# Optimization experiments

Hardware: AMD Instinct MI355X
Metric: run time of the kernel (lower is better)

Reference implementation:

```python
import jax, jax.numpy as jnp
import numpy as np

DIM = 128
P = (2, 2, 2)
D_STATE = 8
D_CONV = 4
EXPAND = 2
D_INNER = EXPAND * DIM
DT_RANK = (DIM + 15) // 16  # ceil(d_model/16) = 8
EPS = 1e-5


def setup_inputs() -> dict:
    key = jax.random.key(0)
    ks = jax.random.split(key, 8)
    B, C, Z, H, W = 2, DIM, 40, 40, 40
    s = lambda k, shape, scale: jax.random.normal(k, shape, jnp.float32) * scale
    return {
        "x": jax.random.normal(ks[0], (B, C, Z, H, W), jnp.float32),
        "norm_g": jnp.ones((C,), jnp.float32),
        "norm_b": jnp.zeros((C,), jnp.float32),
        "in_proj_w": s(ks[1], (2 * D_INNER, C), 0.02),
        "conv_w": s(ks[2], (D_INNER, D_CONV), 0.1),
        "conv_b": jnp.zeros((D_INNER,), jnp.float32),
        "x_proj_w": s(ks[3], (DT_RANK + 2 * D_STATE, D_INNER), 0.02),
        "dt_proj_w": s(ks[4], (D_INNER, DT_RANK), 0.1),
        # softplus^-1(0.01): small positive init for delta, as in mamba_ssm
        "dt_bias": jnp.log(jnp.expm1(jnp.full((D_INNER,), 0.01, jnp.float32))),
        # S4D-real init: A_log = log([1..d_state]) per channel
        "A_log": jnp.log(jnp.tile(jnp.arange(1, D_STATE + 1, dtype=jnp.float32), (D_INNER, 1))),
        "D_vec": jnp.ones((D_INNER,), jnp.float32),
        "out_proj_w": s(ks[5], (DIM, D_INNER), 0.02),
    }


def _mamba(xn, in_proj_w, conv_w, conv_b, x_proj_w, dt_proj_w, dt_bias, A_log, D_vec, out_proj_w):
    # xn: (NB, L, C)
    NB, L, _ = xn.shape
    xz = jnp.einsum('blc,ec->ble', xn, in_proj_w)          # (NB, L, 2*d_inner)
    xp, z = jnp.split(xz, 2, axis=-1)
    # causal depthwise conv1d, kernel D_CONV, truncated to L
    xpad = jnp.pad(xp, ((0, 0), (D_CONV - 1, 0), (0, 0)))
    conv = conv_b
    for k in range(D_CONV):
        conv = conv + xpad[:, k:k + L, :] * conv_w[:, k]
    u = jax.nn.silu(conv)                                  # (NB, L, d_inner)
    xdbl = jnp.einsum('bld,ed->ble', u, x_proj_w)
    dt, Bm, Cm = jnp.split(xdbl, [DT_RANK, DT_RANK + D_STATE], axis=-1)
    delta = jax.nn.softplus(jnp.einsum('blr,dr->bld', dt, dt_proj_w) + dt_bias)
    A = -jnp.exp(A_log)                                    # (d_inner, d_state)

    def step(h, inp):
        d_t, B_t, C_t, u_t = inp  # (NB,d_inner),(NB,d_state),(NB,d_state),(NB,d_inner)
        h = jnp.exp(d_t[:, :, None] * A) * h + (d_t * u_t)[:, :, None] * B_t[:, None, :]
        return h, jnp.einsum('bds,bs->bd', h, C_t)

    h0 = jnp.zeros((NB, D_INNER, D_STATE), xn.dtype)
    xs = (jnp.swapaxes(delta, 0, 1), jnp.swapaxes(Bm, 0, 1),
          jnp.swapaxes(Cm, 0, 1), jnp.swapaxes(u, 0, 1))
    _, ys = jax.lax.scan(step, h0, xs)                     # ys: (L, NB, d_inner)
    y = jnp.swapaxes(ys, 0, 1) + u * D_vec
    y = y * jax.nn.silu(z)
    return jnp.einsum('bld,cd->blc', y, out_proj_w)        # (NB, L, C)


def reference(x, norm_g, norm_b, in_proj_w, conv_w, conv_b, x_proj_w, dt_proj_w,
              dt_bias, A_log, D_vec, out_proj_w):
    B, C, Z, H, W = x.shape
    p1, p2, p3 = P
    NZ, NH, NW = Z // p1, H // p2, W // p3
    NB, L = B * p1 * p2 * p3, NZ * NH * NW
    # patch reshuffle: (B,C,Z,H,W) -> (B*p1*p2*p3, C, NZ, NH, NW)
    xd = x.reshape(B, C, NZ, p1, NH, p2, NW, p3).transpose(0, 3, 5, 7, 1, 2, 4, 6)
    xf = jnp.swapaxes(xd.reshape(NB, C, L), 1, 2)          # (NB, L, C)
    # LayerNorm over channel dim
    mu = xf.mean(-1, keepdims=True)
    var = xf.var(-1, keepdims=True)
    xn = (xf - mu) * jax.lax.rsqrt(var + EPS) * norm_g + norm_b
    yo = _mamba(xn, in_proj_w, conv_w, conv_b, x_proj_w, dt_proj_w, dt_bias,
                A_log, D_vec, out_proj_w)                  # (NB, L, C)
    # undo reshuffle
    xo = jnp.swapaxes(yo, 1, 2).reshape(B, p1, p2, p3, C, NZ, NH, NW)
    xo = xo.transpose(0, 4, 5, 1, 6, 2, 7, 3).reshape(B, C, Z, H, W)
    return xo + x
```

## Files before the change

### kernel.cpp

```cpp
#include <hip/hip_runtime.h>

#define NBATCH 16
#define LSEQ   8000
#define MROWS  128000
#define CDIM   128
#define DI     256
#define DS     8
#define DTR    8
#define NXP    24
#define NC     250
#define CL     32

#define OFF_PB    0ull
#define OFF_XN    1024000ull
#define OFF_STA   1024000ull
#define OFF_XP    33792000ull
#define OFF_XDBL  33792000ull
#define OFF_STH   46080000ull
#define OFF_ZS    99328000ull
#define OFF_U     164864000ull
#define WS_NEEDED 230400000ull

#define P_G    0
#define P_B    128
#define P_IPW  256
#define P_CW   65792
#define P_CB   66816
#define P_XPW  67072
#define P_DTW  73216
#define P_DTB  75264
#define P_ALOG 75520
#define P_DVEC 77568
#define P_OPW  77824
#define P_TOT  110592

typedef __attribute__((ext_vector_type(8))) short bf16x8;
typedef __attribute__((ext_vector_type(4))) float f32x4;
typedef __attribute__((ext_vector_type(2))) float f32x2;

__device__ __forceinline__ float bf2f(unsigned short a) {
    union { unsigned int u; float f; } v; v.u = ((unsigned int)a) << 16; return v.f;
}
__device__ __forceinline__ unsigned short f2bf(float f) {
    union { float f; unsigned int u; } v; v.f = f;
    unsigned int r = v.u + 0x7FFFu + ((v.u >> 16) & 1u);
    return (unsigned short)(r >> 16);
}
__device__ __forceinline__ unsigned short f2bf_cvt(float f) {
    unsigned int r;
    asm("v_cvt_pk_bf16_f32 %0, %1, %2" : "=v"(r) : "v"(f), "v"(0.f));
    return (unsigned short)r;
}
__device__ __forceinline__ bool bfmode(const void* g) {
    return ((const unsigned int*)g)[0] == 0x3F803F80u;
}
__device__ __forceinline__ float rd(const void* p, size_t i, bool bf) {
    return bf ? bf2f(((const unsigned short*)p)[i]) : ((const float*)p)[i];
}
__device__ __forceinline__ f32x2 pk_fma(f32x2 a, f32x2 b, f32x2 c) {
    f32x2 d;
    asm("v_pk_fma_f32 %0, %1, %2, %3" : "=v"(d) : "v"(a), "v"(b), "v"(c));
    return d;
}
__device__ __forceinline__ f32x2 pk_mul(f32x2 a, f32x2 b) {
    f32x2 d;
    asm("v_pk_mul_f32 %0, %1, %2" : "=v"(d) : "v"(a), "v"(b));
    return d;
}
__device__ __forceinline__ int m_of(int b, int sp) {
    int z = sp / 1600;
    int rem = sp - z * 1600;
    int h = rem / 40;
    int w = rem - h * 40;
    int nb = b * 8 + (z & 1) * 4 + (h & 1) * 2 + (w & 1);
    int l = (z >> 1) * 400 + (h >> 1) * 20 + (w >> 1);
    return nb * LSEQ + l;
}

__global__ __launch_bounds__(256) void param_convert(const void* g, const void* b, const void* ipw,
                                                     const void* cw, const void* cb, const void* xpw,
                                                     const void* dtw, const void* dtb, const void* alog,
                                                     const void* dvec, const void* opw,
                                                     unsigned short* __restrict__ pb)
{
    int gid = blockIdx.x * 256 + threadIdx.x;
    if (gid >= P_TOT) return;
    bool bf = bfmode(g);
    const void* src; int off;
    if      (gid < P_B)    { src = g;    off = P_G; }
    else if (gid < P_IPW)  { src = b;    off = P_B; }
    else if (gid < P_CW)   { src = ipw;  off = P_IPW; }
    else if (gid < P_CB)   { src = cw;   off = P_CW; }
    else if (gid < P_XPW)  { src = cb;   off = P_CB; }
    else if (gid < P_DTW)  { src = xpw;  off = P_XPW; }
    else if (gid < P_DTB)  { src = dtw;  off = P_DTW; }
    else if (gid < P_ALOG) { src = dtb;  off = P_DTB; }
    else if (gid < P_DVEC) { src = alog; off = P_ALOG; }
    else if (gid < P_OPW)  { src = dvec; off = P_DVEC; }
    else                   { src = opw;  off = P_OPW; }
    pb[gid] = f2bf(rd(src, gid - off, bf));
}

__global__ __launch_bounds__(256) void lnorm_kernel(const void* __restrict__ x,
                                                    const unsigned short* __restrict__ pb,
                                                    unsigned short* __restrict__ xn)
{
    __shared__ float tile[128][65];
    __shared__ float psum[4][64], psqs[4][64];
    __shared__ float smu[64], srs[64];
    int b  = blockIdx.y;
    int sp0 = blockIdx.x * 64;
    int t = threadIdx.x;

    int spi = t & 63, cpart = t >> 6;
    const float* xf = (const float*)x;
#pragma unroll
    for (int pass = 0; pass < 32; ++pass) {
        int c = pass * 4 + cpart;
        tile[c][spi] = xf[((size_t)b * CDIM + c) * 64000 + sp0 + spi];
    }
    __syncthreads();

    {
        float s = 0.f, ss = 0.f;
        int c0 = cpart * 32;
#pragma unroll
        for (int cc = 0; cc < 32; ++cc) {
            float v = tile[c0 + cc][spi];
            s += v; ss += v * v;
        }
        psum[cpart][spi] = s; psqs[cpart][spi] = ss;
    }
    __syncthreads();
    if (cpart == 0) {
        float s  = psum[0][spi] + psum[1][spi] + psum[2][spi] + psum[3][spi];
        float ss = psqs[0][spi] + psqs[1][spi] + psqs[2][spi] + psqs[3][spi];
        float m = s * (1.f / CDIM);
        float var = ss * (1.f / CDIM) - m * m;
        smu[spi] = m;
        srs[spi] = rsqrtf(var + 1e-5f);
    }
    __syncthreads();

    int c = t & 127, half = t >> 7;
    float gc = bf2f(pb[P_G + c]), bc = bf2f(pb[P_B + c]);
#pragma unroll
    for (int pass = 0; pass < 32; ++pass) {
        int j = pass * 2 + half;
        int m = m_of(b, sp0 + j);
        float v = (tile[c][j] - smu[j]) * srs[j] * gc + bc;
        xn[(size_t)m * CDIM + c] = f2bf(v);
    }
}

__global__ __launch_bounds__(256) void gemm_bt_kernel(const unsigned short* __restrict__ A,
                                                      const unsigned short* __restrict__ W,
                                                      void* __restrict__ D,
                                                      int K, int Nact, int ldd, int act)
{
    __shared__ unsigned short As[128 * 32];
    __shared__ unsigned short Ws[128 * 32];
    int tid = threadIdx.x;
    int m0 = blockIdx.x * 128;
    int n0 = blockIdx.y * 128;
    int wave = tid >> 6, lane = tid & 63;
    int wm = (wave & 1) * 64, wn = (wave >> 1) * 64;
    int lrow = lane & 15, lk = (lane >> 4) * 8;
    int quad = lane >> 4;

    f32x4 acc[4][4];
#pragma unroll
    for (int i = 0; i < 4; i++)
#pragma unroll
        for (int j = 0; j < 4; j++) acc[i][j] = (f32x4){0.f, 0.f, 0.f, 0.f};

    int rowA0 = tid >> 2, kcA0 = (tid & 3) << 3;
    int rowA1 = (tid + 256) >> 2, kcA1 = (tid & 3) << 3;

    for (int kt = 0; kt < K; kt += 32) {
        *(uint4*)&As[rowA0 * 32 + kcA0] = *(const uint4*)&A[(size_t)(m0 + rowA0) * K + kt + kcA0];
        *(uint4*)&As[rowA1 * 32 + kcA1] = *(const uint4*)&A[(size_t)(m0 + rowA1) * K + kt + kcA1];
        uint4 z4 = {0u, 0u, 0u, 0u};
        uint4 w0 = (n0 + rowA0 < Nact) ? *(const uint4*)&W[(size_t)(n0 + rowA0) * K + kt + kcA0] : z4;
        uint4 w1 = (n0 + rowA1 < Nact) ? *(const uint4*)&W[(size_t)(n0 + rowA1) * K + kt + kcA1] : z4;
        *(uint4*)&Ws[rowA0 * 32 + kcA0] = w0;
        *(uint4*)&Ws[rowA1 * 32 + kcA1] = w1;
        __syncthreads();

        bf16x8 af[4], bfr[4];
#pragma unroll
        for (int i = 0; i < 4; i++) af[i]  = *(const bf16x8*)&As[(wm + i * 16 + lrow) * 32 + lk];
#pragma unroll
        for (int j = 0; j < 4; j++) bfr[j] = *(const bf16x8*)&Ws[(wn + j * 16 + lrow) * 32 + lk];
#pragma unroll
        for (int i = 0; i < 4; i++)
#pragma unroll
            for (int j = 0; j < 4; j++)
                acc[i][j] = __builtin_amdgcn_mfma_f32_16x16x32_bf16(af[i], bfr[j], acc[i][j], 0, 0, 0);
        __syncthreads();
    }

#pragma unroll
    for (int i = 0; i < 4; i++)
#pragma unroll
        for (int j = 0; j < 4; j++) {
            int n = n0 + wn + j * 16 + lrow;
            if (n < Nact) {
#pragma unroll
                for (int r = 0; r < 4; r++) {
                    int m = m0 + wm + i * 16 + quad * 4 + r;
                    float v = acc[i][j][r];
                    if (act == 1) v = v / (1.f + __expf(-v));
                    ((unsigned short*)D)[(size_t)m * ldd + n] = f2bf(v);
                }
            }
        }
}

__global__ __launch_bounds__(256) void gemm_conv_kernel(const unsigned short* __restrict__ A,
                                                        const unsigned short* __restrict__ W,
                                                        const unsigned short* __restrict__ cw,
                                                        const unsigned short* __restrict__ cb,
                                                        unsigned short* __restrict__ u)
{
    __shared__ unsigned short As[128 * 32];
    __shared__ unsigned short Ws[128 * 32];
    __shared__ unsigned short Dt[128 * 132];

    int tid = threadIdx.x;
    int tile = blockIdx.x & 63;
    int nb = blockIdx.x >> 6;
    int n0 = blockIdx.y * 128;
    int m0 = nb * 8000 + tile * 125;
    int mA = m0 - 3;
    int wave = tid >> 6, lane = tid & 63;
    int wm = (wave & 1) * 64, wn = (wave >> 1) * 64;
    int lrow = lane & 15, lk = (lane >> 4) * 8;
    int quad = lane >> 4;

    f32x4 acc[4][4];
#pragma unroll
    for (int i = 0; i < 4; i++)
#pragma unroll
        for (int j = 0; j < 4; j++) acc[i][j] = (f32x4){0.f, 0.f, 0.f, 0.f};

    int rowA0 = tid >> 2, kcA0 = (tid & 3) << 3;
    int rowA1 = (tid + 256) >> 2;

    for (int kt = 0; kt < CDIM; kt += 32) {
        uint4 z4 = {0u, 0u, 0u, 0u};
        uint4 a0 = (tile == 0 && rowA0 < 3) ? z4
                 : *(const uint4*)&A[(size_t)(mA + rowA0) * CDIM + kt + kcA0];
        uint4 a1 = *(const uint4*)&A[(size_t)(mA + rowA1) * CDIM + kt + kcA0];
        *(uint4*)&As[rowA0 * 32 + kcA0] = a0;
        *(uint4*)&As[rowA1 * 32 + kcA0] = a1;
        *(uint4*)&Ws[rowA0 * 32 + kcA0] = *(const uint4*)&W[(size_t)(n0 + rowA0) * CDIM + kt + kcA0];
        *(uint4*)&Ws[rowA1 * 32 + kcA0] = *(const uint4*)&W[(size_t)(n0 + rowA1) * CDIM + kt + kcA0];
        __syncthreads();

        bf16x8 af[4], bfr[4];
#pragma unroll
        for (int i = 0; i < 4; i++) af[i]  = *(const bf16x8*)&As[(wm + i * 16 + lrow) * 32 + lk];
#pragma unroll
        for (int j = 0; j < 4; j++) bfr[j] = *(const bf16x8*)&Ws[(wn + j * 16 + lrow) * 32 + lk];
#pragma unroll
        for (int i = 0; i < 4; i++)
#pragma unroll
            for (int j = 0; j < 4; j++)
                acc[i][j] = __builtin_amdgcn_mfma_f32_16x16x32_bf16(af[i], bfr[j], acc[i][j], 0, 0, 0);
        __syncthreads();
    }

#pragma unroll
    for (int i = 0; i < 4; i++)
#pragma unroll
        for (int j = 0; j < 4; j++) {
            int nl = wn + j * 16 + lrow;
            int tr = wm + i * 16 + quad * 4;
            unsigned int c01, c23;
            asm("v_cvt_pk_bf16_f32 %0, %1, %2" : "=v"(c01) : "v"(acc[i][j][0]), "v"(acc[i][j][1]));
            asm("v_cvt_pk_bf16_f32 %0, %1, %2" : "=v"(c23) : "v"(acc[i][j][2]), "v"(acc[i][j][3]));
            *(unsigned int*)&Dt[nl * 132 + tr]     = c01;
            *(unsigned int*)&Dt[nl * 132 + tr + 2] = c23;
        }
    __syncthreads();

    {
        int nl = tid & 127, half = tid >> 7;
        int dch = n0 + nl;
        float cw0 = bf2f(cw[dch * 4 + 0]), cw1 = bf2f(cw[dch * 4 + 1]);
        float cw2 = bf2f(cw[dch * 4 + 2]), cw3 = bf2f(cw[dch * 4 + 3]);
        float cbv = bf2f(cb[dch]);
        int tr0 = half ? 66 : 3;
        int nsteps = half ? 62 : 63;
        const unsigned short* col = &Dt[nl * 132];
        float x0 = bf2f(col[tr0 - 3]), x1 = bf2f(col[tr0 - 2]), x2 = bf2f(col[tr0 - 1]);
        unsigned short* uout = &u[(size_t)(m0 + tr0 - 3) * DI + dch];
#pragma unroll 1
        for (int k = 0; k < nsteps; ++k) {
            float x3 = bf2f(col[tr0 + k]);
            float a = cbv + cw0 * x0 + cw1 * x1 + cw2 * x2 + cw3 * x3;
            float uv = a * __builtin_amdgcn_rcpf(1.f + __expf(-a));
            *uout = f2bf_cvt(uv);
            uout += DI;
            x0 = x1; x1 = x2; x2 = x3;
        }
    }
}


#define BODY1(UR, RO) do {                                                       \
    union { f32x4 q; f32x2 h[2]; } qa, qb, qc, qd;                               \
    qa.q = *(const f32x4*)(rfp + (RO));                                          \
    qb.q = *(const f32x4*)(rfp + (RO) + 4);                                      \
    qc.q = *(const f32x4*)(rfp + (RO) + 8);                                      \
    qd.q = *(const f32x4*)(rfp + (RO) + 12);                                     \
    f32x2 din2 = pk_fma(qa.h[0], Wq[0], bias2);                                  \
    din2 = pk_fma(qa.h[1], Wq[1], din2);                                         \
    din2 = pk_fma(qb.h[0], Wq[2], din2);                                         \
    din2 = pk_fma(qb.h[1], Wq[3], din2);                                         \
    float din = din2.x + din2.y;                                                 \
    float e = __expf(din);                                                       \
    float w = 1.f + e;                                                           \
    float p1 = __builtin_amdgcn_rcpf(w);                                         \
    float delta = (din > 15.f) ? din : __logf(w);                                \
    float du = delta * bf2f(UR);                                                 \
    float p2 = p1 * p1;                                                          \
    f32x2 q1; q1.x = p1; q1.y = p2;                                              \
    f32x2 pp2; pp2.x = p2; pp2.y = p2;                                           \
    f32x2 q2 = pk_mul(q1, pp2);                                                  \
    f32x2 pp4; pp4.x = q2.y; pp4.y = q2.y;                                       \
    f32x2 q3 = pk_mul(q1, pp4);                                                  \
    f32x2 q4 = pk_mul(q2, pp4);                                                  \
    f32x2 du2; du2.x = du; du2.y = du;                                           \
    h2[0] = pk_fma(du2, qc.h[0], pk_mul(q1, h2[0]));                             \
    h2[1] = pk_fma(du2, qc.h[1], pk_mul(q2, h2[1]));                             \
    h2[2] = pk_fma(du2, qd.h[0], pk_mul(q3, h2[2]));                             \
    h2[3] = pk_fma(du2, qd.h[1], pk_mul(q4, h2[3]));                             \
    P *= p1;                                                                     \
} while (0)

__global__ __launch_bounds__(256) void gemm_xdbl_scan1(const unsigned short* __restrict__ u,
                                                       const unsigned short* __restrict__ W,
                                                       const unsigned short* __restrict__ dtw,
                                                       const unsigned short* __restrict__ dtb,
                                                       const unsigned short* __restrict__ alog,
                                                       float* __restrict__ xdbl,
                                                       float* __restrict__ stA,
                                                       float* __restrict__ stH)
{
    __shared__ unsigned short As[128 * 32];
    __shared__ unsigned short Ws[128 * 32];
    __shared__ float Dxs[128 * NXP];
    int tid = threadIdx.x;
    int m0 = blockIdx.x * 128;
    int wave = tid >> 6, lane = tid & 63;
    int wm = (wave & 1) * 64, wn = (wave >> 1) * 64;
    int lrow = lane & 15, lk = (lane >> 4) * 8;
    int quad = lane >> 4;

    f32x4 acc[4][4];
#pragma unroll
    for (int i = 0; i < 4; i++)
#pragma unroll
        for (int j = 0; j < 4; j++) acc[i][j] = (f32x4){0.f, 0.f, 0.f, 0.f};

    int rowA0 = tid >> 2, kcA0 = (tid & 3) << 3;
    int rowA1 = (tid + 256) >> 2;

    for (int kt = 0; kt < DI; kt += 32) {
        *(uint4*)&As[rowA0 * 32 + kcA0] = *(const uint4*)&u[(size_t)(m0 + rowA0) * DI + kt + kcA0];
        *(uint4*)&As[rowA1 * 32 + kcA0] = *(const uint4*)&u[(size_t)(m0 + rowA1) * DI + kt + kcA0];
        uint4 z4 = {0u, 0u, 0u, 0u};
        uint4 w0 = (rowA0 < NXP) ? *(const uint4*)&W[(size_t)rowA0 * DI + kt + kcA0] : z4;
        *(uint4*)&Ws[rowA0 * 32 + kcA0] = w0;
        *(uint4*)&Ws[rowA1 * 32 + kcA0] = z4;
        __syncthreads();

        bf16x8 af[4], bfr[4];
#pragma unroll
        for (int i = 0; i < 4; i++) af[i]  = *(const bf16x8*)&As[(wm + i * 16 + lrow) * 32 + lk];
#pragma unroll
        for (int j = 0; j < 4; j++) bfr[j] = *(const bf16x8*)&Ws[(wn + j * 16 + lrow) * 32 + lk];
#pragma unroll
        for (int i = 0; i < 4; i++)
#pragma unroll
            for (int j = 0; j < 4; j++)
                acc[i][j] = __builtin_amdgcn_mfma_f32_16x16x32_bf16(af[i], bfr[j], acc[i][j], 0, 0, 0);
        __syncthreads();
    }

#pragma unroll
    for (int i = 0; i < 4; i++)
#pragma unroll
        for (int j = 0; j < 4; j++) {
            int n = wn + j * 16 + lrow;
            if (n < NXP) {
#pragma unroll
                for (int r = 0; r < 4; r++) {
                    int ml = wm + i * 16 + quad * 4 + r;
                    float v = acc[i][j][r];
                    xdbl[(size_t)(m0 + ml) * NXP + n] = v;
                    Dxs[ml * NXP + n] = v;
                }
            }
        }
    __syncthreads();

    int d = tid;
    f32x2 Wq[4];
#pragma unroll
    for (int r = 0; r < 4; r++) {
        Wq[r].x = bf2f(dtw[d * DTR + 2 * r]);
        Wq[r].y = bf2f(dtw[d * DTR + 2 * r + 1]);
    }
    float Av[DS];
#pragma unroll
    for (int s = 0; s < DS; s++) Av[s] = -__expf(bf2f(alog[d * DS + s]));
    float A1 = Av[0];
    bool fast = (A1 == -1.0f);
#pragma unroll
    for (int s = 1; s < DS; s++)
        fast = fast && (fabsf(Av[s] - (float)(s + 1) * A1) <= 0.02f * (float)(s + 1) * fabsf(A1));
    float bias = bf2f(dtb[d]);
    f32x2 bias2; bias2.x = bias; bias2.y = 0.f;

#pragma unroll 1
    for (int k = 0; k < 4; ++k) {
        int gm0 = m0 + 32 * k;
        int nb = gm0 / 8000;
        int cc = (gm0 - nb * 8000) >> 5;
        size_t o = (((size_t)cc * NBATCH + nb) * DI + d) * DS;
        const unsigned short* up = u + (size_t)gm0 * DI + d;
        const float* rfp = &Dxs[32 * k * NXP];

        if (fast) {
            f32x2 h2[4];
#pragma unroll
            for (int i = 0; i < 4; i++) { h2[i].x = 0.f; h2[i].y = 0.f; }
            float P = 1.f;
            unsigned short u0 = up[0], u1 = up[DI];
            const unsigned short* uld = up + 2 * DI;
#pragma unroll 1
            for (int t = 0; t < CL - 2; t += 2) {
                unsigned short ua = uld[0], ub = uld[DI]; uld += 2 * DI;
                BODY1(u0, 0);
                BODY1(u1, NXP);
                u0 = ua; u1 = ub;
                rfp += 2 * NXP;
            }
            BODY1(u0, 0);
            BODY1(u1, NXP);
            float P2 = P * P, P3 = P2 * P, P4 = P2 * P2;
            float apv[DS] = {P, P2, P3, P4, P4 * P, P3 * P3, P4 * P3, P4 * P4};
#pragma unroll
            for (int s = 0; s < DS; s++) stA[o + s] = apv[s];
#pragma unroll
            for (int i = 0; i < 4; i++) { stH[o + 2 * i] = h2[i].x; stH[o + 2 * i + 1] = h2[i].y; }
        } else {
            float Wdt[DTR];
#pragma unroll
            for (int r = 0; r < 4; r++) { Wdt[2 * r] = Wq[r].x; Wdt[2 * r + 1] = Wq[r].y; }
            float h[DS], ap[DS];
#pragma unroll
            for (int s = 0; s < DS; s++) { h[s] = 0.f; ap[s] = 1.f; }
            const unsigned short* uld = up;
#pragma unroll 1
            for (int t = 0; t < CL; ++t) {
                float uv = bf2f(*uld); uld += DI;
                float din = bias;
#pragma unroll
                for (int r = 0; r < DTR; r++) din += rfp[r] * Wdt[r];
                float delta = (din > 15.f) ? din : __logf(1.f + __expf(din));
                float du = delta * uv;
#pragma unroll
                for (int s = 0; s < DS; s++) {
                    float dA = __expf(delta * Av[s]);
                    h[s] = dA * h[s] + du * rfp[8 + s];
                    ap[s] *= dA;
                }
                rfp += NXP;
            }
#pragma unroll
            for (int s = 0; s < DS; s++) { stA[o + s] = ap[s]; stH[o + s] = h[s]; }
        }
    }
}

__global__ __launch_bounds__(256) void scan_phase2(float* __restrict__ stA, float* __restrict__ stH)
{
    size_t t = blockIdx.x * 256 + threadIdx.x;
    const size_t stride = (size_t)NBATCH * DI * DS;
    float hin = 0.f;
    size_t idx = t;
    float a[10], hl[10], an[10], hn[10];
#pragma unroll
    for (int j = 0; j < 10; ++j) { a[j] = stA[idx + j * stride]; hl[j] = stH[idx + j * stride]; }
#pragma unroll 1
    for (int g = 0; g < 25; ++g) {
        size_t nidx = idx + 10 * stride;
        if (g < 24) {
#pragma unroll
            for (int j = 0; j < 10; ++j) { an[j] = stA[nidx + j * stride]; hn[j] = stH[nidx + j * stride]; }
        }
#pragma unroll
        for (int j = 0; j < 10; ++j) {
            stH[idx + j * stride] = hin;
            hin = a[j] * hin + hl[j];
        }
#pragma unroll
        for (int j = 0; j < 10; ++j) { a[j] = an[j]; hl[j] = hn[j]; }
        idx = nidx;
    }
}

#define BODY3(UR, ZR, RO, ZO) do {                                               \
    union { f32x4 q; f32x2 h[2]; } qa, qb, qc, qd, qe, qf;                       \
    qa.q = *(const f32x4*)(rfp + (RO));                                          \
    qb.q = *(const f32x4*)(rfp + (RO) + 4);                                      \
    qc.q = *(const f32x4*)(rfp + (RO) + 8);                                      \
    qd.q = *(const f32x4*)(rfp + (RO) + 12);                                     \
    qe.q = *(const f32x4*)(rfp + (RO) + 16);                                     \
    qf.q = *(const f32x4*)(rfp + (RO) + 20);                                     \
    f32x2 din2 = pk_fma(qa.h[0], Wq[0], bias2);                                  \
    din2 = pk_fma(qa.h[1], Wq[1], din2);                                         \
    din2 = pk_fma(qb.h[0], Wq[2], din2);                                         \
    din2 = pk_fma(qb.h[1], Wq[3], din2);                                         \
    float din = din2.x + din2.y;                                                 \
    float e = __expf(din);                                                       \
    float w = 1.f + e;                                                           \
    float p1 = __builtin_amdgcn_rcpf(w);                                         \
    float delta = (din > 15.f) ? din : __logf(w);                                \
    float uv = bf2f(UR);                                                         \
    float du = delta * uv;                                                       \
    float p2 = p1 * p1;                                                          \
    f32x2 q1; q1.x = p1; q1.y = p2;                                              \
    f32x2 pp2; pp2.x = p2; pp2.y = p2;                                           \
    f32x2 q2 = pk_mul(q1, pp2);                                                  \
    f32x2 pp4; pp4.x = q2.y; pp4.y = q2.y;                                       \
    f32x2 q3 = pk_mul(q1, pp4);                                                  \
    f32x2 q4 = pk_mul(q2, pp4);                                                  \
    f32x2 du2; du2.x = du; du2.y = du;                                           \
    h2[0] = pk_fma(du2, qc.h[0], pk_mul(q1, h2[0]));                             \
    h2[1] = pk_fma(du2, qc.h[1], pk_mul(q2, h2[1]));                             \
    h2[2] = pk_fma(du2, qd.h[0], pk_mul(q3, h2[2]));                             \
    h2[3] = pk_fma(du2, qd.h[1], pk_mul(q4, h2[3]));                             \
    f32x2 y2v = pk_mul(h2[0], qe.h[0]);                                          \
    y2v = pk_fma(h2[1], qe.h[1], y2v);                                           \
    y2v = pk_fma(h2[2], qf.h[0], y2v);                                           \
    y2v = pk_fma(h2[3], qf.h[1], y2v);                                           \
    float y = __builtin_fmaf(uv, Dv, y2v.x) + y2v.y;                             \
    zw[ZO] = f2bf_cvt(y * bf2f(ZR));                                             \
} while (0)

__global__ __launch_bounds__(256) void scan_phase3(unsigned short* __restrict__ zs,
                                                   const unsigned short* __restrict__ u,
                                                   const float* __restrict__ xdbl,
                                                   const unsigned short* __restrict__ dtw,
                                                   const unsigned short* __restrict__ dtb,
                                                   const unsigned short* __restrict__ alog,
                                                   const unsigned short* __restrict__ dvec,
                                                   const float* __restrict__ stH)
{
    __shared__ float xs[CL * NXP];
    int c = blockIdx.x, nb = blockIdx.y, d = threadIdx.x;
    size_t base = (size_t)nb * LSEQ + (size_t)c * CL;
    {
        const uint4* src = (const uint4*)(xdbl + base * NXP);
        uint4* dst = (uint4*)xs;
        int tt = threadIdx.x;
        if (tt < 192) dst[tt] = src[tt];
    }
    float Av[DS];
    f32x2 Wq[4];
#pragma unroll
    for (int r = 0; r < 4; r++) {
        Wq[r].x = bf2f(dtw[d * DTR + 2 * r]);
        Wq[r].y = bf2f(dtw[d * DTR + 2 * r + 1]);
    }
#pragma unroll
    for (int s = 0; s < DS; s++) Av[s] = -__expf(bf2f(alog[d * DS + s]));
    float A1 = Av[0];
    bool fast = (A1 == -1.0f);
#pragma unroll
    for (int s = 1; s < DS; s++)
        fast = fast && (fabsf(Av[s] - (float)(s + 1) * A1) <= 0.02f * (float)(s + 1) * fabsf(A1));
    float bias = bf2f(dtb[d]);
    f32x2 bias2; bias2.x = bias; bias2.y = 0.f;
    float Dv = bf2f(dvec[d]);
    size_t o = (((size_t)c * NBATCH + nb) * DI + d) * DS;
    const unsigned short* up = u + base * DI + d;
    unsigned short* zp = zs + base * DI + d;
    __syncthreads();

    if (fast) {
        f32x2 h2[4];
#pragma unroll
        for (int i = 0; i < 4; i++) { h2[i].x = stH[o + 2 * i]; h2[i].y = stH[o + 2 * i + 1]; }
        const float* rfp = xs;
        unsigned short u0 = up[0], u1 = up[DI];
        unsigned short z0 = zp[0], z1 = zp[DI];
        const unsigned short* uld = up + 2 * DI;
        const unsigned short* zld = zp + 2 * DI;
        unsigned short* zw = zp;
#pragma unroll 1
        for (int t = 0; t < CL - 2; t += 2) {
            unsigned short ua = uld[0], ub = uld[DI]; uld += 2 * DI;
            unsigned short za = zld[0], zb = zld[DI]; zld += 2 * DI;
            BODY3(u0, z0, 0, 0);
            BODY3(u1, z1, NXP, DI);
            u0 = ua; u1 = ub; z0 = za; z1 = zb;
            zw += 2 * DI; rfp += 2 * NXP;
        }
        BODY3(u0, z0, 0, 0);
        BODY3(u1, z1, NXP, DI);
    } else {
        float Wdt[DTR];
#pragma unroll
        for (int r = 0; r < 4; r++) { Wdt[2 * r] = Wq[r].x; Wdt[2 * r + 1] = Wq[r].y; }
        float h[DS];
#pragma unroll
        for (int s = 0; s < DS; s++) h[s] = stH[o + s];
        const float* rfp = xs;
        const unsigned short* uld = up;
        unsigned short* zw = zp;
#pragma unroll 1
        for (int t = 0; t < CL; ++t) {
            float uv = bf2f(*uld); uld += DI;
            float szv = bf2f(*zw);
            float din = bias;
#pragma unroll
            for (int r = 0; r < DTR; r++) din += rfp[r] * Wdt[r];
            float delta = (din > 15.f) ? din : __logf(1.f + __expf(din));
            float du = delta * uv;
            float y = 0.f;
#pragma unroll
            for (int s = 0; s < DS; s++) {
                float dA = __expf(delta * Av[s]);
                h[s] = dA * h[s] + du * rfp[8 + s];
                y += h[s] * rfp[16 + s];
            }
            y += uv * Dv;
            *zw = f2bf(y * szv);
            zw += DI;
            rfp += NXP;
        }
    }
}

__global__ __launch_bounds__(256) void unpatch_kernel(const void* __restrict__ x,
                                                      const unsigned short* __restrict__ y2,
                                                      float* __restrict__ out)
{
    __shared__ float ytile[64][129];
    int b  = blockIdx.y;
    int sp0 = blockIdx.x * 64;
    int t = threadIdx.x;

    {
        int c = t & 127, half = t >> 7;
#pragma unroll
        for (int pass = 0; pass < 32; ++pass) {
            int j = pass * 2 + half;
            int m = m_of(b, sp0 + j);
            ytile[j][c] = bf2f(y2[(size_t)m * CDIM + c]);
        }
    }
    __syncthreads();

    const float* xf = (const float*)x;
    int spi = t & 63, cpart = t >> 6;
#pragma unroll
    for (int pass = 0; pass < 32; ++pass) {
        int c = pass * 4 + cpart;
        size_t idx = ((size_t)b * CDIM + c) * 64000 + sp0 + spi;
        out[idx] = xf[idx] + ytile[spi][c];
    }
}

extern "C" void kernel_launch(void* const* d_in, const int* in_sizes, int n_in,
                              void* d_out, int out_size, void* d_ws, size_t ws_size,
                              hipStream_t stream)
{
    const void* x     = d_in[0];
    const void* ng    = d_in[1];
    const void* nb_   = d_in[2];
    const void* ipw   = d_in[3];
    const void* cw    = d_in[4];
    const void* cb    = d_in[5];
    const void* xpw   = d_in[6];
    const void* dtw   = d_in[7];
    const void* dtb   = d_in[8];
    const void* alog  = d_in[9];
    const void* dvec  = d_in[10];
    const void* opw   = d_in[11];
    float* out = (float*)d_out;

    if (ws_size < WS_NEEDED) return;

    char* ws = (char*)d_ws;
    unsigned short* pb   = (unsigned short*)(ws + OFF_PB);
    unsigned short* xn   = (unsigned short*)(ws + OFF_XN);
    float* stA = (float*)(ws + OFF_STA);
    float* stH = (float*)(ws + OFF_STH);
    float* xdblf = (float*)(ws + OFF_XDBL);
    unsigned short* zs   = (unsigned short*)(ws + OFF_ZS);
    unsigned short* u    = (unsigned short*)(ws + OFF_U);
    unsigned short* y2   = xn;

    param_convert<<<432, 256, 0, stream>>>(ng, nb_, ipw, cw, cb, xpw, dtw, dtb, alog, dvec, opw, pb);
    lnorm_kernel<<<dim3(1000, 2), 256, 0, stream>>>(x, pb, xn);
    gemm_conv_kernel<<<dim3(1024, 2), 256, 0, stream>>>(xn, pb + P_IPW, pb + P_CW, pb + P_CB, u);
    gemm_bt_kernel<<<dim3(1000, 2), 256, 0, stream>>>(xn, pb + P_IPW + 256 * 128, zs, CDIM, DI, DI, 1);
    gemm_xdbl_scan1<<<dim3(1000, 1), 256, 0, stream>>>(u, pb + P_XPW, pb + P_DTW, pb + P_DTB,
                                                       pb + P_ALOG, xdblf, stA, stH);
    scan_phase2<<<128, 256, 0, stream>>>(stA, stH);
    scan_phase3<<<dim3(NC, NBATCH), 256, 0, stream>>>(zs, u, xdblf, pb + P_DTW, pb + P_DTB,
                                                      pb + P_ALOG, pb + P_DVEC, stH);
    gemm_bt_kernel<<<dim3(1000, 1), 256, 0, stream>>>(zs, pb + P_OPW, y2, DI, CDIM, CDIM, 0);
    unpatch_kernel<<<dim3(1000, 2), 256, 0, stream>>>(x, y2, out);
}
```

Measured before the change: 398.6 us.

## Fuse scan phase 3 with output projection GEMM and shrink xdbl tiles

The phase-3 scan now writes its gated output into a shared-memory tile, and the same block then runs the out_proj MFMA GEMM on those 32 rows. This removes the zs write-back and the separate output GEMM launch. The xdbl GEMM+scan1 kernel also moves from 128-row to 64-row tiles with a smaller 32-column weight tile, which doubles the grid and cuts wasted MFMA work on the padded N dimension. In exchange, out_proj weights are read from global memory by every block, and the fused kernel uses more shared memory.

```diff
diff --git a/kernel.cpp b/kernel.cpp
--- a/kernel.cpp
+++ b/kernel.cpp
@@ -349,62 +349,54 @@
                                                        float* __restrict__ stA,
                                                        float* __restrict__ stH)
 {
-    __shared__ unsigned short As[128 * 32];
-    __shared__ unsigned short Ws[128 * 32];
-    __shared__ float Dxs[128 * NXP];
+    __shared__ unsigned short As[64 * 32];
+    __shared__ unsigned short Ws[32 * 32];
+    __shared__ float Dxs[64 * NXP];
     int tid = threadIdx.x;
-    int m0 = blockIdx.x * 128;
+    int m0 = blockIdx.x * 64;
     int wave = tid >> 6, lane = tid & 63;
-    int wm = (wave & 1) * 64, wn = (wave >> 1) * 64;
+    int wm = (wave & 1) * 32, wn = (wave >> 1) * 16;
     int lrow = lane & 15, lk = (lane >> 4) * 8;
     int quad = lane >> 4;
 
-    f32x4 acc[4][4];
-#pragma unroll
-    for (int i = 0; i < 4; i++)
-#pragma unroll
-        for (int j = 0; j < 4; j++) acc[i][j] = (f32x4){0.f, 0.f, 0.f, 0.f};
-
-    int rowA0 = tid >> 2, kcA0 = (tid & 3) << 3;
-    int rowA1 = (tid + 256) >> 2;
+    f32x4 acc[2];
+    acc[0] = (f32x4){0.f, 0.f, 0.f, 0.f};
+    acc[1] = (f32x4){0.f, 0.f, 0.f, 0.f};
+
+    int rowA = tid >> 2, kcA = (tid & 3) << 3;
 
     for (int kt = 0; kt < DI; kt += 32) {
-        *(uint4*)&As[rowA0 * 32 + kcA0] = *(const uint4*)&u[(size_t)(m0 + rowA0) * DI + kt + kcA0];
-        *(uint4*)&As[rowA1 * 32 + kcA0] = *(const uint4*)&u[(size_t)(m0 + rowA1) * DI + kt + kcA0];
-        uint4 z4 = {0u, 0u, 0u, 0u};
-        uint4 w0 = (rowA0 < NXP) ? *(const uint4*)&W[(size_t)rowA0 * DI + kt + kcA0] : z4;
-        *(uint4*)&Ws[rowA0 * 32 + kcA0] = w0;
-        *(uint4*)&Ws[rowA1 * 32 + kcA0] = z4;
+        *(uint4*)&As[rowA * 32 + kcA] = *(const uint4*)&u[(size_t)(m0 + rowA) * DI + kt + kcA];
+        if (tid < 128) {
+            uint4 z4 = {0u, 0u, 0u, 0u};
+            int rw = tid >> 2;
+            uint4 w0 = (rw < NXP) ? *(const uint4*)&W[(size_t)rw * DI + kt + kcA] : z4;
+            *(uint4*)&Ws[rw * 32 + kcA] = w0;
+        }
         __syncthreads();
 
-        bf16x8 af[4], bfr[4];
-#pragma unroll
-        for (int i = 0; i < 4; i++) af[i]  = *(const bf16x8*)&As[(wm + i * 16 + lrow) * 32 + lk];
-#pragma unroll
-        for (int j = 0; j < 4; j++) bfr[j] = *(const bf16x8*)&Ws[(wn + j * 16 + lrow) * 32 + lk];
-#pragma unroll
-        for (int i = 0; i < 4; i++)
-#pragma unroll
-            for (int j = 0; j < 4; j++)
-                acc[i][j] = __builtin_amdgcn_mfma_f32_16x16x32_bf16(af[i], bfr[j], acc[i][j], 0, 0, 0);
+        bf16x8 af0 = *(const bf16x8*)&As[(wm + lrow) * 32 + lk];
+        bf16x8 af1 = *(const bf16x8*)&As[(wm + 16 + lrow) * 32 + lk];
+        bf16x8 bfr = *(const bf16x8*)&Ws[(wn + lrow) * 32 + lk];
+        acc[0] = __builtin_amdgcn_mfma_f32_16x16x32_bf16(af0, bfr, acc[0], 0, 0, 0);
+        acc[1] = __builtin_amdgcn_mfma_f32_16x16x32_bf16(af1, bfr, acc[1], 0, 0, 0);
         __syncthreads();
     }
 
-#pragma unroll
-    for (int i = 0; i < 4; i++)
-#pragma unroll
-        for (int j = 0; j < 4; j++) {
-            int n = wn + j * 16 + lrow;
-            if (n < NXP) {
+    {
+        int n = wn + lrow;
+        if (n < NXP) {
+#pragma unroll
+            for (int i = 0; i < 2; i++)
 #pragma unroll
                 for (int r = 0; r < 4; r++) {
                     int ml = wm + i * 16 + quad * 4 + r;
-                    float v = acc[i][j][r];
+                    float v = acc[i][r];
                     xdbl[(size_t)(m0 + ml) * NXP + n] = v;
                     Dxs[ml * NXP + n] = v;
                 }
-            }
-        }
+        }
+    }
     __syncthreads();
 
     int d = tid;
@@ -426,7 +418,7 @@
     f32x2 bias2; bias2.x = bias; bias2.y = 0.f;
 
 #pragma unroll 1
-    for (int k = 0; k < 4; ++k) {
+    for (int k = 0; k < 2; ++k) {
         int gm0 = m0 + 32 * k;
         int nb = gm0 / 8000;
         int cc = (gm0 - nb * 8000) >> 5;
@@ -514,7 +506,7 @@
     }
 }
 
-#define BODY3(UR, ZR, RO, ZO) do {                                               \
+#define BODY3Y(UR, ZR, RO, T) do {                                               \
     union { f32x4 q; f32x2 h[2]; } qa, qb, qc, qd, qe, qf;                       \
     qa.q = *(const f32x4*)(rfp + (RO));                                          \
     qb.q = *(const f32x4*)(rfp + (RO) + 4);                                      \
@@ -550,34 +542,40 @@
     y2v = pk_fma(h2[2], qf.h[0], y2v);                                           \
     y2v = pk_fma(h2[3], qf.h[1], y2v);                                           \
     float y = __builtin_fmaf(uv, Dv, y2v.x) + y2v.y;                             \
-    zw[ZO] = f2bf_cvt(y * bf2f(ZR));                                             \
+    ytcol[(T) * 264] = f2bf_cvt(y * bf2f(ZR));                                   \
 } while (0)
 
-__global__ __launch_bounds__(256) void scan_phase3(unsigned short* __restrict__ zs,
-                                                   const unsigned short* __restrict__ u,
-                                                   const float* __restrict__ xdbl,
-                                                   const unsigned short* __restrict__ dtw,
-                                                   const unsigned short* __restrict__ dtb,
-                                                   const unsigned short* __restrict__ alog,
-                                                   const unsigned short* __restrict__ dvec,
-                                                   const float* __restrict__ stH)
+__global__ __launch_bounds__(256) void scan3_gemm_out(const unsigned short* __restrict__ zs,
+                                                      const unsigned short* __restrict__ u,
+                                                      const float* __restrict__ xdbl,
+                                                      const unsigned short* __restrict__ dtw,
+                                                      const unsigned short* __restrict__ dtb,
+                                                      const unsigned short* __restrict__ alog,
+                                                      const unsigned short* __restrict__ dvec,
+                                                      const float* __restrict__ stH,
+                                                      const unsigned short* __restrict__ W,
+                                                      unsigned short* __restrict__ y2)
 {
     __shared__ float xs[CL * NXP];
-    int c = blockIdx.x, nb = blockIdx.y, d = threadIdx.x;
-    size_t base = (size_t)nb * LSEQ + (size_t)c * CL;
+    __shared__ unsigned short Yt[CL * 264];
+    int tid = threadIdx.x;
+    int gm0 = blockIdx.x * 32;
+    int nb = gm0 / 8000;
+    int c  = (gm0 - nb * 8000) >> 5;
+    int d = tid;
+    size_t base = (size_t)gm0;
     {
         const uint4* src = (const uint4*)(xdbl + base * NXP);
         uint4* dst = (uint4*)xs;
-        int tt = threadIdx.x;
-        if (tt < 192) dst[tt] = src[tt];
-    }
-    float Av[DS];
+        if (tid < 192) dst[tid] = src[tid];
+    }
     f32x2 Wq[4];
 #pragma unroll
     for (int r = 0; r < 4; r++) {
         Wq[r].x = bf2f(dtw[d * DTR + 2 * r]);
         Wq[r].y = bf2f(dtw[d * DTR + 2 * r + 1]);
     }
+    float Av[DS];
 #pragma unroll
     for (int s = 0; s < DS; s++) Av[s] = -__expf(bf2f(alog[d * DS + s]));
     float A1 = Av[0];
@@ -590,7 +588,8 @@
     float Dv = bf2f(dvec[d]);
     size_t o = (((size_t)c * NBATCH + nb) * DI + d) * DS;
     const unsigned short* up = u + base * DI + d;
-    unsigned short* zp = zs + base * DI + d;
+    const unsigned short* zp = zs + base * DI + d;
+    unsigned short* ytcol = &Yt[d];
     __syncthreads();
 
     if (fast) {
@@ -602,18 +601,17 @@
         unsigned short z0 = zp[0], z1 = zp[DI];
         const unsigned short* uld = up + 2 * DI;
         const unsigned short* zld = zp + 2 * DI;
-        unsigned short* zw = zp;
 #pragma unroll 1
         for (int t = 0; t < CL - 2; t += 2) {
             unsigned short ua = uld[0], ub = uld[DI]; uld += 2 * DI;
             unsigned short za = zld[0], zb = zld[DI]; zld += 2 * DI;
-            BODY3(u0, z0, 0, 0);
-            BODY3(u1, z1, NXP, DI);
+            BODY3Y(u0, z0, 0, t);
+            BODY3Y(u1, z1, NXP, t + 1);
             u0 = ua; u1 = ub; z0 = za; z1 = zb;
-            zw += 2 * DI; rfp += 2 * NXP;
-        }
-        BODY3(u0, z0, 0, 0);
-        BODY3(u1, z1, NXP, DI);
+            rfp += 2 * NXP;
+        }
+        BODY3Y(u0, z0, 0, CL - 2);
+        BODY3Y(u1, z1, NXP, CL - 1);
     } else {
         float Wdt[DTR];
 #pragma unroll
@@ -623,11 +621,11 @@
         for (int s = 0; s < DS; s++) h[s] = stH[o + s];
         const float* rfp = xs;
         const unsigned short* uld = up;
-        unsigned short* zw = zp;
+        const unsigned short* zld = zp;
 #pragma unroll 1
         for (int t = 0; t < CL; ++t) {
             float uv = bf2f(*uld); uld += DI;
-            float szv = bf2f(*zw);
+            float szv = bf2f(*zld); zld += DI;
             float din = bias;
 #pragma unroll
             for (int r = 0; r < DTR; r++) din += rfp[r] * Wdt[r];
@@ -641,10 +639,49 @@
                 y += h[s] * rfp[16 + s];
             }
             y += uv * Dv;
-            *zw = f2bf(y * szv);
-            zw += DI;
+            ytcol[t * 264] = f2bf_cvt(y * szv);
             rfp += NXP;
         }
+    }
+    __syncthreads();
+
+    {
+        int wave = tid >> 6, lane = tid & 63;
+        int wn = wave * 32;
+        int lrow = lane & 15, lk = (lane >> 4) * 8;
+        int quad = lane >> 4;
+        f32x4 acc[2][2];
+#pragma unroll
+        for (int i = 0; i < 2; i++)
+#pragma unroll
+            for (int j = 0; j < 2; j++) acc[i][j] = (f32x4){0.f, 0.f, 0.f, 0.f};
+
+        for (int kt = 0; kt < DI; kt += 32) {
+            bf16x8 af[2], bfr[2];
+#pragma unroll
+            for (int i = 0; i < 2; i++)
+                af[i] = *(const bf16x8*)&Yt[(i * 16 + lrow) * 264 + kt + lk];
+#pragma unroll
+            for (int j = 0; j < 2; j++)
+                bfr[j] = *(const bf16x8*)&W[(size_t)(wn + j * 16 + lrow) * DI + kt + lk];
+#pragma unroll
+            for (int i = 0; i < 2; i++)
+#pragma unroll
+                for (int j = 0; j < 2; j++)
+                    acc[i][j] = __builtin_amdgcn_mfma_f32_16x16x32_bf16(af[i], bfr[j], acc[i][j], 0, 0, 0);
+        }
+
+#pragma unroll
+        for (int i = 0; i < 2; i++)
+#pragma unroll
+            for (int j = 0; j < 2; j++) {
+                int n = wn + j * 16 + lrow;
+#pragma unroll
+                for (int r = 0; r < 4; r++) {
+                    int m = i * 16 + quad * 4 + r;
+                    y2[(size_t)(gm0 + m) * CDIM + n] = f2bf_cvt(acc[i][j][r]);
+                }
+            }
     }
 }
 
@@ -712,11 +749,10 @@
     lnorm_kernel<<<dim3(1000, 2), 256, 0, stream>>>(x, pb, xn);
     gemm_conv_kernel<<<dim3(1024, 2), 256, 0, stream>>>(xn, pb + P_IPW, pb + P_CW, pb + P_CB, u);
     gemm_bt_kernel<<<dim3(1000, 2), 256, 0, stream>>>(xn, pb + P_IPW + 256 * 128, zs, CDIM, DI, DI, 1);
-    gemm_xdbl_scan1<<<dim3(1000, 1), 256, 0, stream>>>(u, pb + P_XPW, pb + P_DTW, pb + P_DTB,
-                                                       pb + P_ALOG, xdblf, stA, stH);
+    gemm_xdbl_scan1<<<2000, 256, 0, stream>>>(u, pb + P_XPW, pb + P_DTW, pb + P_DTB,
+                                              pb + P_ALOG, xdblf, stA, stH);
     scan_phase2<<<128, 256, 0, stream>>>(stA, stH);
-    scan_phase3<<<dim3(NC, NBATCH), 256, 0, stream>>>(zs, u, xdblf, pb + P_DTW, pb + P_DTB,
-                                                      pb + P_ALOG, pb + P_DVEC, stH);
-    gemm_bt_kernel<<<dim3(1000, 1), 256, 0, stream>>>(zs, pb + P_OPW, y2, DI, CDIM, CDIM, 0);
+    scan3_gemm_out<<<4000, 256, 0, stream>>>(zs, u, xdblf, pb + P_DTW, pb + P_DTB,
+                                             pb + P_ALOG, pb + P_DVEC, stH, pb + P_OPW, y2);
     unpatch_kernel<<<dim3(1000, 2), 256, 0, stream>>>(x, y2, out);
 }
```

New measurement: 373.9 us. -6.2%, faster.
